# Kernel optimization log

Measured on AMD Instinct MI355X. Metric: run time of the kernel, lower is better.

Reference implementation:

```python
import jax, jax.numpy as jnp
import numpy as np

N = 20000      # nodes
E = 320000     # edges (avg degree 16)
D = 256        # in_dim == embed_dim
L = 4          # num_layers
G = 128        # number of graphs in the batch
OUT = 64       # out_dim


def setup_inputs() -> dict:
    key = jax.random.key(0)
    ks = jax.random.split(key, 10)
    s = 1.0 / np.sqrt(D)
    x = jax.random.normal(ks[0], (N, D), jnp.float32)
    edge_src = jax.random.randint(ks[1], (E,), 0, N, jnp.int32)
    edge_dst = jax.random.randint(ks[2], (E,), 0, N, jnp.int32)
    batch_ids = jnp.sort(jax.random.randint(ks[3], (N,), 0, G, jnp.int32))
    W1 = jax.random.uniform(ks[4], (L, D, D), jnp.float32, -s, s)
    b1 = jax.random.uniform(ks[5], (L, D), jnp.float32, -s, s)
    W2 = jax.random.uniform(ks[6], (L, D, D), jnp.float32, -s, s)
    b2 = jax.random.uniform(ks[7], (L, D), jnp.float32, -s, s)
    Wout = jax.random.uniform(ks[8], (D, OUT), jnp.float32, -s, s)
    bout = jax.random.uniform(ks[9], (OUT,), jnp.float32, -s, s)
    return {"x": x, "edge_src": edge_src, "edge_dst": edge_dst,
            "batch_ids": batch_ids, "W1": W1, "b1": b1, "W2": W2,
            "b2": b2, "Wout": Wout, "bout": bout}


def reference(x, edge_src, edge_dst, batch_ids, W1, b1, W2, b2, Wout, bout):
    n = x.shape[0]
    h = x
    num_layers = W1.shape[0]
    for i in range(num_layers):
        # GINConv: (1+eps)*x + sum-aggregate of neighbor messages (eps=0)
        agg = jax.ops.segment_sum(h[edge_src], edge_dst, num_segments=n)
        z = h + agg
        # GINConv MLP: Linear -> ReLU -> Linear (plain last)
        z = jnp.maximum(z @ W1[i] + b1[i], 0.0) @ W2[i] + b2[i]
        # BasicGNN inter-layer activation (skipped after last layer, jk=None)
        h = jnp.maximum(z, 0.0) if i < num_layers - 1 else z
    # global_add_pool over graph segment ids
    pooled = jax.ops.segment_sum(h, batch_ids, num_segments=G)  # [G, D]
    out = pooled @ Wout + bout  # [G, OUT]
    return (out, pooled)
```

## Files before the change

### kernel.cpp

```cpp
#include <hip/hip_runtime.h>

#define DIM 256
#define DOUT 64
#define PSPLITS 16

typedef short bf16x8 __attribute__((ext_vector_type(8)));
typedef float f32x4 __attribute__((ext_vector_type(4)));
typedef unsigned short u16x8 __attribute__((ext_vector_type(8)));

static __device__ __forceinline__ float b2f(unsigned short u) {
    return __uint_as_float(((unsigned)u) << 16);
}
static __device__ __forceinline__ unsigned short f2bf(float f) {
    unsigned u = __float_as_uint(f);
    unsigned r = (u + 0x7fffu + ((u >> 16) & 1u)) >> 16;
    return (unsigned short)r;
}

__global__ void cvt_f32_bf16(const float4* __restrict__ src, ushort4* __restrict__ dst, int n4) {
    int i = blockIdx.x * blockDim.x + threadIdx.x;
    int stride = gridDim.x * blockDim.x;
    for (; i < n4; i += stride) {
        float4 v = src[i];
        ushort4 o;
        o.x = f2bf(v.x); o.y = f2bf(v.y); o.z = f2bf(v.z); o.w = f2bf(v.w);
        dst[i] = o;
    }
}

__global__ void hist_kernel(const int* __restrict__ dst, int* __restrict__ deg, int E) {
    int i = blockIdx.x * blockDim.x + threadIdx.x;
    if (i < E) atomicAdd(&deg[dst[i]], 1);
}

__global__ void scan_blocksum(const int* __restrict__ deg, int* __restrict__ bsum, int n) {
    __shared__ int s[256];
    int t = threadIdx.x;
    int i = blockIdx.x * 256 + t;
    s[t] = (i < n) ? deg[i] : 0;
    __syncthreads();
    for (int off = 128; off > 0; off >>= 1) {
        if (t < off) s[t] += s[t + off];
        __syncthreads();
    }
    if (t == 0) bsum[blockIdx.x] = s[0];
}

__global__ void scan_partials(int* __restrict__ bsum, int* __restrict__ row_ptr,
                              int nb, int n) {
    __shared__ int s[256];
    int t = threadIdx.x;
    int v = (t < nb) ? bsum[t] : 0;
    s[t] = v;
    __syncthreads();
    for (int off = 1; off < 256; off <<= 1) {
        int u = (t >= off) ? s[t - off] : 0;
        __syncthreads();
        s[t] += u;
        __syncthreads();
    }
    if (t < nb) bsum[t] = s[t] - v;
    if (t == 255) row_ptr[n] = s[255];
}

__global__ void scan_final(int* __restrict__ deg, int* __restrict__ row_ptr,
                           const int* __restrict__ bsum, int n) {
    __shared__ int s[256];
    int t = threadIdx.x;
    int i = blockIdx.x * 256 + t;
    int d = (i < n) ? deg[i] : 0;
    s[t] = d;
    __syncthreads();
    for (int off = 1; off < 256; off <<= 1) {
        int u = (t >= off) ? s[t - off] : 0;
        __syncthreads();
        s[t] += u;
        __syncthreads();
    }
    if (i < n) {
        int val = bsum[blockIdx.x] + s[t] - d;
        row_ptr[i] = val;
        deg[i] = val;
    }
}

__global__ void scatter_kernel(const int* __restrict__ src, const int* __restrict__ dst,
                               int* __restrict__ cursor, int* __restrict__ perm, int E) {
    int i = blockIdx.x * blockDim.x + threadIdx.x;
    if (i < E) {
        int d = dst[i];
        int p = atomicAdd(&cursor[d], 1);
        perm[p] = src[i];
    }
}

__global__ void transpose_w(const float* __restrict__ W, unsigned short* __restrict__ Wt) {
    __shared__ float tile[32][33];
    int l = blockIdx.z;
    int k0 = blockIdx.x * 32, n0 = blockIdx.y * 32;
    const float* Wl = W + (size_t)l * DIM * DIM;
    unsigned short* Wtl = Wt + (size_t)l * DIM * DIM;
    int tx = threadIdx.x, ty = threadIdx.y;
    for (int i = ty; i < 32; i += 8)
        tile[i][tx] = Wl[(size_t)(k0 + i) * DIM + n0 + tx];
    __syncthreads();
    for (int i = ty; i < 32; i += 8)
        Wtl[(size_t)(n0 + i) * DIM + k0 + tx] = f2bf(tile[tx][i]);
}

__global__ void agg_kernel(const unsigned short* __restrict__ H, const int* __restrict__ row_ptr,
                           const int* __restrict__ perm, unsigned short* __restrict__ Z, int n) {
    int wave = threadIdx.x >> 6;
    int lane = threadIdx.x & 63;
    int node = blockIdx.x * 4 + wave;
    if (node >= n) return;
    const int half = lane >> 5;
    const int sl = lane & 31;
    const u16x8* hb = (const u16x8*)H;
    float acc[8];
    {
        u16x8 own = hb[(size_t)node * 32 + sl];
#pragma unroll
        for (int q = 0; q < 8; ++q) acc[q] = half ? 0.f : b2f(own[q]);
    }
    const int lo = row_ptr[node], hi = row_ptr[node + 1];
    int e = lo + half;
    for (; e + 14 < hi; e += 16) {
        u16x8 v[8];
#pragma unroll
        for (int j = 0; j < 8; ++j)
            v[j] = hb[(size_t)perm[e + 2 * j] * 32 + sl];
#pragma unroll
        for (int j = 0; j < 8; ++j)
#pragma unroll
            for (int q = 0; q < 8; ++q) acc[q] += b2f(v[j][q]);
    }
    for (; e + 6 < hi; e += 8) {
        u16x8 v[4];
#pragma unroll
        for (int j = 0; j < 4; ++j)
            v[j] = hb[(size_t)perm[e + 2 * j] * 32 + sl];
#pragma unroll
        for (int j = 0; j < 4; ++j)
#pragma unroll
            for (int q = 0; q < 8; ++q) acc[q] += b2f(v[j][q]);
    }
    for (; e < hi; e += 2) {
        u16x8 v = hb[(size_t)perm[e] * 32 + sl];
#pragma unroll
        for (int q = 0; q < 8; ++q) acc[q] += b2f(v[q]);
    }
#pragma unroll
    for (int q = 0; q < 8; ++q) acc[q] += __shfl_xor(acc[q], 32);
    if (half == 0) {
        u16x8 o;
#pragma unroll
        for (int q = 0; q < 8; ++q) o[q] = f2bf(acc[q]);
        ((u16x8*)Z)[(size_t)node * 32 + sl] = o;
    }
}

template <bool RELU>
__global__ __launch_bounds__(256, 2) void mfma_gemm(const unsigned short* __restrict__ A,
                                                    const unsigned short* __restrict__ Bt,
                                                    const float* __restrict__ bias,
                                                    unsigned short* __restrict__ C, int M) {
    __shared__ unsigned short Bs[128 * 256];
    const int tid = threadIdx.x;
    const int wave = tid >> 6;
    const int lane = tid & 63;
    const int l15 = lane & 15;
    const int g4 = lane >> 4;
    const int half = blockIdx.x & 1;
    const int mslice = blockIdx.x >> 1;
    const int NT = (M + 15) / 16;

    {
        const char* gsrc = (const char*)&Bt[(size_t)half * 128 * 256];
#pragma unroll
        for (int jj = 0; jj < 16; ++jj) {
            int chunk = tid + jj * 256;
            int col = chunk >> 5;
            int kbyte = (chunk & 31) * 16;
            *reinterpret_cast<u16x8*>((char*)Bs + col * 512 + (kbyte ^ ((col & 7) << 4))) =
                *reinterpret_cast<const u16x8*>(gsrc + col * 512 + kbyte);
        }
    }
    __syncthreads();

    bf16x8 b[4][8];
#pragma unroll
    for (int n = 0; n < 4; ++n) {
        const int col = (wave & 1) * 64 + n * 16 + l15;
        const char* cbase = (const char*)Bs + col * 512;
        const int sw = (col & 7) << 4;
#pragma unroll
        for (int k8 = 0; k8 < 8; ++k8) {
            int kbyte = (k8 * 32 + g4 * 8) * 2;
            b[n][k8] = *reinterpret_cast<const bf16x8*>(cbase + (kbyte ^ sw));
        }
    }

    const int ncol0 = half * 128 + (wave & 1) * 64;
    float bv[4];
#pragma unroll
    for (int n = 0; n < 4; ++n) bv[n] = bias[ncol0 + n * 16 + l15];

    const int base = mslice * 2 + (wave >> 1);

    auto loadA = [&](bf16x8 (&a)[8], int t) {
        int r = t * 16 + l15;
        if (r >= M) r = M - 1;
        const unsigned short* arow = &A[(size_t)r * 256];
#pragma unroll
        for (int k8 = 0; k8 < 8; ++k8)
            a[k8] = *reinterpret_cast<const bf16x8*>(arow + k8 * 32 + g4 * 8);
    };

    auto computeStore = [&](bf16x8 (&a)[8], int t) {
        f32x4 acc[4] = {};
#pragma unroll
        for (int k8 = 0; k8 < 8; ++k8)
#pragma unroll
            for (int n = 0; n < 4; ++n)
                acc[n] = __builtin_amdgcn_mfma_f32_16x16x32_bf16(a[k8], b[n][k8], acc[n], 0, 0, 0);
        int r0 = t * 16 + g4 * 4;
#pragma unroll
        for (int n = 0; n < 4; ++n) {
            int col = ncol0 + n * 16 + l15;
#pragma unroll
            for (int r = 0; r < 4; ++r) {
                int row = r0 + r;
                if (row < M) {
                    float v = acc[n][r] + bv[n];
                    if (RELU) v = fmaxf(v, 0.f);
                    C[(size_t)row * 256 + col] = f2bf(v);
                }
            }
        }
    };

    bf16x8 a0[8], a1[8];
    int t = base;
    if (t >= NT) return;
    loadA(a0, t);
#pragma unroll 1
    for (int rep = 0; rep < 2; ++rep) {
        if (t >= NT) break;
        if (t + 512 < NT) loadA(a1, t + 512);
        computeStore(a0, t);
        t += 512;
        if (t >= NT) break;
        if (t + 512 < NT) loadA(a0, t + 512);
        computeStore(a1, t);
        t += 512;
    }
}

__global__ void gstart_kernel(const int* __restrict__ bids, int* __restrict__ gstart,
                              int n, int G) {
    int g = blockIdx.x * blockDim.x + threadIdx.x;
    if (g > G) return;
    if (g == G) { gstart[G] = n; return; }
    int lo = 0, hi = n;
    while (lo < hi) {
        int mid = (lo + hi) >> 1;
        if (bids[mid] < g) lo = mid + 1; else hi = mid;
    }
    gstart[g] = lo;
}

__global__ void pool_kernel(const ushort4* __restrict__ h4, const int* __restrict__ gstart,
                            float* __restrict__ pooled) {
    int g = blockIdx.x;
    int split = blockIdx.y;
    int lane = threadIdx.x;
    int lo = gstart[g], hi = gstart[g + 1];
    int cnt = hi - lo;
    int chunk = (cnt + PSPLITS - 1) / PSPLITS;
    int s0 = lo + split * chunk;
    int s1 = min(s0 + chunk, hi);
    if (s0 >= s1) return;
    float ax = 0.f, ay = 0.f, az = 0.f, aw = 0.f;
    for (int nd = s0; nd < s1; ++nd) {
        ushort4 v = h4[(size_t)nd * 64 + lane];
        ax += b2f(v.x); ay += b2f(v.y); az += b2f(v.z); aw += b2f(v.w);
    }
    float* p = &pooled[(size_t)g * DIM + lane * 4];
    atomicAdd(p + 0, ax);
    atomicAdd(p + 1, ay);
    atomicAdd(p + 2, az);
    atomicAdd(p + 3, aw);
}

__global__ void final_kernel(const float* __restrict__ Tp, const int* __restrict__ gstart,
                             const float* __restrict__ W2, const float* __restrict__ b2,
                             const float* __restrict__ Wout, const float* __restrict__ bout,
                             float* __restrict__ out, float* __restrict__ pooled) {
    __shared__ float tps[DIM];
    __shared__ float pl[DIM];
    int g = blockIdx.x;
    int tidx = threadIdx.x;
    float cnt = (float)(gstart[g + 1] - gstart[g]);
    tps[tidx] = Tp[(size_t)g * DIM + tidx];
    __syncthreads();
    float acc = cnt * b2[tidx];
    for (int d = 0; d < DIM; ++d)
        acc += tps[d] * W2[(size_t)d * DIM + tidx];
    pooled[(size_t)g * DIM + tidx] = acc;
    pl[tidx] = acc;
    __syncthreads();
    if (tidx < DOUT) {
        float o = bout[tidx];
        for (int d = 0; d < DIM; ++d)
            o += pl[d] * Wout[(size_t)d * DOUT + tidx];
        out[(size_t)g * DOUT + tidx] = o;
    }
}

extern "C" void kernel_launch(void* const* d_in, const int* in_sizes, int n_in,
                              void* d_out, int out_size, void* d_ws, size_t ws_size,
                              hipStream_t stream) {
    const float* x    = (const float*)d_in[0];
    const int*   esrc = (const int*)d_in[1];
    const int*   edst = (const int*)d_in[2];
    const int*   bids = (const int*)d_in[3];
    const float* W1   = (const float*)d_in[4];
    const float* b1   = (const float*)d_in[5];
    const float* W2   = (const float*)d_in[6];
    const float* b2   = (const float*)d_in[7];
    const float* Wout = (const float*)d_in[8];
    const float* bout = (const float*)d_in[9];

    const int N = in_sizes[3];
    const int E = in_sizes[1];
    const int L = in_sizes[5] / DIM;
    const int G = out_size / (DOUT + DIM);
    const int NB = (N + 255) / 256;

    char* ws = (char*)d_ws;
    size_t off = 0;
    auto carve = [&](size_t bytes) -> char* {
        char* p = ws + off;
        off = (off + bytes + 255) & ~(size_t)255;
        return p;
    };
    int* row_ptr = (int*)carve((size_t)(N + 1) * sizeof(int));
    int* cursor  = (int*)carve((size_t)N * sizeof(int));
    int* perm    = (int*)carve((size_t)E * sizeof(int));
    int* gstart  = (int*)carve((size_t)(G + 1) * sizeof(int));
    int* bsum    = (int*)carve((size_t)256 * sizeof(int));
    float* Tp    = (float*)carve((size_t)G * DIM * sizeof(float));
    unsigned short* h   = (unsigned short*)carve((size_t)N * DIM * 2);
    unsigned short* z   = (unsigned short*)carve((size_t)N * DIM * 2);
    unsigned short* t   = (unsigned short*)carve((size_t)N * DIM * 2);
    unsigned short* wt1 = (unsigned short*)carve((size_t)L * DIM * DIM * 2);
    unsigned short* wt2 = (unsigned short*)carve((size_t)L * DIM * DIM * 2);
    (void)ws_size;

    cvt_f32_bf16<<<2048, 256, 0, stream>>>((const float4*)x, (ushort4*)h, N * (DIM / 4));

    hipMemsetAsync(cursor, 0, (size_t)N * sizeof(int), stream);
    hist_kernel<<<(E + 255) / 256, 256, 0, stream>>>(edst, cursor, E);
    scan_blocksum<<<NB, 256, 0, stream>>>(cursor, bsum, N);
    scan_partials<<<1, 256, 0, stream>>>(bsum, row_ptr, NB, N);
    scan_final<<<NB, 256, 0, stream>>>(cursor, row_ptr, bsum, N);
    scatter_kernel<<<(E + 255) / 256, 256, 0, stream>>>(esrc, edst, cursor, perm, E);

    {
        dim3 tgrid(DIM / 32, DIM / 32, L);
        dim3 tblk(32, 8);
        transpose_w<<<tgrid, tblk, 0, stream>>>(W1, wt1);
        transpose_w<<<tgrid, tblk, 0, stream>>>(W2, wt2);
    }

    for (int l = 0; l < L; ++l) {
        agg_kernel<<<(N + 3) / 4, 256, 0, stream>>>(h, row_ptr, perm, z, N);
        mfma_gemm<true><<<512, 256, 0, stream>>>(
            z, wt1 + (size_t)l * DIM * DIM, b1 + (size_t)l * DIM, t, N);
        if (l < L - 1)
            mfma_gemm<true><<<512, 256, 0, stream>>>(
                t, wt2 + (size_t)l * DIM * DIM, b2 + (size_t)l * DIM, h, N);
    }

    float* outp   = (float*)d_out;
    float* pooled = outp + (size_t)G * DOUT;
    hipMemsetAsync(Tp, 0, (size_t)G * DIM * sizeof(float), stream);
    gstart_kernel<<<1, 256, 0, stream>>>(bids, gstart, N, G);
    {
        dim3 pgrid(G, PSPLITS);
        pool_kernel<<<pgrid, 64, 0, stream>>>((const ushort4*)t, gstart, Tp);
    }
    final_kernel<<<G, 256, 0, stream>>>(Tp, gstart,
                                        W2 + (size_t)(L - 1) * DIM * DIM,
                                        b2 + (size_t)(L - 1) * DIM,
                                        Wout, bout, outp, pooled);
}
```

Measured before the change: 255.9 us.

## Fuse the two GIN MLP GEMMs into a producer/consumer warp-specialized kernel

For the first three layers, the separate Linear1 and Linear2 GEMM launches are replaced by one kernel. In it, four producer waves compute ReLU(Z·W1+b1) for 32-row tiles into double-buffered swizzled LDS, and four consumer waves compute ReLU(·W2+b2) from LDS and write H. Each wave keeps its 64-column weight slice in registers. This removes the global write and reread of the intermediate activation t and one launch per layer. The costs are heavy register use (32 bf16x8 B fragments per wave), per-tile __syncthreads, and uncoalesced scalar 2-byte stores of H.

```diff
diff --git a/kernel.cpp b/kernel.cpp
--- a/kernel.cpp
+++ b/kernel.cpp
@@ -158,6 +158,108 @@
         for (int q = 0; q < 8; ++q) o[q] = f2bf(acc[q]);
         ((u16x8*)Z)[(size_t)node * 32 + sl] = o;
     }
+}
+
+__global__ __launch_bounds__(512, 2) void fused_mlp_pc(
+        const unsigned short* __restrict__ Z,
+        const unsigned short* __restrict__ Wt1, const float* __restrict__ b1,
+        const unsigned short* __restrict__ Wt2, const float* __restrict__ b2,
+        unsigned short* __restrict__ H, int M) {
+    __shared__ unsigned char lds[32768];
+    const int tid = threadIdx.x;
+    const int wave = tid >> 6;
+    const int lane = tid & 63;
+    const int l15 = lane & 15;
+    const int g4 = lane >> 4;
+    const bool producer = wave < 4;
+    const int p = wave & 3;
+    const int NT = (M + 31) / 32;
+
+    const unsigned short* Wt = producer ? Wt1 : Wt2;
+    const float* bias = producer ? b1 : b2;
+    bf16x8 b[4][8];
+#pragma unroll
+    for (int n = 0; n < 4; ++n) {
+        const unsigned short* cbase = Wt + (size_t)(p * 64 + n * 16 + l15) * 256;
+#pragma unroll
+        for (int k8 = 0; k8 < 8; ++k8)
+            b[n][k8] = *reinterpret_cast<const bf16x8*>(cbase + k8 * 32 + g4 * 8);
+    }
+    float bv[4];
+#pragma unroll
+    for (int n = 0; n < 4; ++n) bv[n] = bias[p * 64 + n * 16 + l15];
+
+    auto prodTile = [&](int t32, char* base) {
+#pragma unroll
+        for (int h16 = 0; h16 < 2; ++h16) {
+            int r = t32 * 32 + h16 * 16 + l15;
+            if (r >= M) r = M - 1;
+            const unsigned short* arow = Z + (size_t)r * 256;
+            bf16x8 a[8];
+#pragma unroll
+            for (int k8 = 0; k8 < 8; ++k8)
+                a[k8] = *reinterpret_cast<const bf16x8*>(arow + k8 * 32 + g4 * 8);
+            f32x4 acc[4] = {};
+#pragma unroll
+            for (int k8 = 0; k8 < 8; ++k8)
+#pragma unroll
+                for (int n = 0; n < 4; ++n)
+                    acc[n] = __builtin_amdgcn_mfma_f32_16x16x32_bf16(a[k8], b[n][k8],
+                                                                     acc[n], 0, 0, 0);
+#pragma unroll
+            for (int n = 0; n < 4; ++n) {
+                int col2 = (p * 64 + n * 16 + l15) * 2;
+#pragma unroll
+                for (int rr = 0; rr < 4; ++rr) {
+                    int row = h16 * 16 + g4 * 4 + rr;
+                    *(unsigned short*)(base + row * 512 + (col2 ^ ((row & 7) << 4))) =
+                        f2bf(fmaxf(acc[n][rr] + bv[n], 0.f));
+                }
+            }
+        }
+    };
+
+    auto consTile = [&](int t32, char* base) {
+#pragma unroll
+        for (int h16 = 0; h16 < 2; ++h16) {
+            int rl = h16 * 16 + l15;
+            int sw = (rl & 7) << 4;
+            bf16x8 a[8];
+#pragma unroll
+            for (int k8 = 0; k8 < 8; ++k8)
+                a[k8] = *reinterpret_cast<const bf16x8*>(
+                    base + rl * 512 + ((k8 * 64 + g4 * 16) ^ sw));
+            f32x4 acc[4] = {};
+#pragma unroll
+            for (int k8 = 0; k8 < 8; ++k8)
+#pragma unroll
+                for (int n = 0; n < 4; ++n)
+                    acc[n] = __builtin_amdgcn_mfma_f32_16x16x32_bf16(a[k8], b[n][k8],
+                                                                     acc[n], 0, 0, 0);
+            int r0 = t32 * 32 + h16 * 16 + g4 * 4;
+#pragma unroll
+            for (int n = 0; n < 4; ++n) {
+                int col = p * 64 + n * 16 + l15;
+#pragma unroll
+                for (int rr = 0; rr < 4; ++rr) {
+                    int row = r0 + rr;
+                    if (row < M)
+                        H[(size_t)row * 256 + col] = f2bf(fmaxf(acc[n][rr] + bv[n], 0.f));
+                }
+            }
+        }
+    };
+
+    int prev = -1;
+    int buf = 0;
+    for (int t32 = blockIdx.x; t32 < NT; t32 += gridDim.x) {
+        if (producer) prodTile(t32, (char*)lds + buf * 16384);
+        else if (prev >= 0) consTile(prev, (char*)lds + (buf ^ 1) * 16384);
+        __syncthreads();
+        prev = t32;
+        buf ^= 1;
+    }
+    if (!producer && prev >= 0) consTile(prev, (char*)lds + (buf ^ 1) * 16384);
 }
 
 template <bool RELU>
@@ -376,11 +478,13 @@
 
     for (int l = 0; l < L; ++l) {
         agg_kernel<<<(N + 3) / 4, 256, 0, stream>>>(h, row_ptr, perm, z, N);
-        mfma_gemm<true><<<512, 256, 0, stream>>>(
-            z, wt1 + (size_t)l * DIM * DIM, b1 + (size_t)l * DIM, t, N);
         if (l < L - 1)
+            fused_mlp_pc<<<256, 512, 0, stream>>>(
+                z, wt1 + (size_t)l * DIM * DIM, b1 + (size_t)l * DIM,
+                wt2 + (size_t)l * DIM * DIM, b2 + (size_t)l * DIM, h, N);
+        else
             mfma_gemm<true><<<512, 256, 0, stream>>>(
-                t, wt2 + (size_t)l * DIM * DIM, b2 + (size_t)l * DIM, h, N);
+                z, wt1 + (size_t)l * DIM * DIM, b1 + (size_t)l * DIM, t, N);
     }
 
     float* outp   = (float*)d_out;
```

Result: slower. 265.2 us (+3.6%).
